# Optimization experiments

Measured on AMD Instinct MI355X. Metric: run time of the kernel, lower is better.

## Reference

```python
import jax, jax.numpy as jnp
import numpy as np

N = 50000   # nodes
E = 600000  # edges
D = 128     # in_channels
H = 32      # MLP hidden


def setup_inputs() -> dict:
    key = jax.random.key(0)
    ks = jax.random.split(key, 10)
    x = jax.random.normal(ks[0], (N, D), dtype=jnp.float32)
    edge_index = jax.random.randint(ks[1], (2, E), 0, N, dtype=jnp.int32)
    W_gcn = jax.random.normal(ks[2], (D, D), dtype=jnp.float32) / np.sqrt(D)
    b_gcn = jnp.zeros((D,), dtype=jnp.float32)
    w1 = jax.random.normal(ks[3], (D, H), dtype=jnp.float32) / np.sqrt(D)
    b1 = jnp.zeros((H,), dtype=jnp.float32)
    w2 = jax.random.normal(ks[4], (H, H), dtype=jnp.float32) / np.sqrt(H)
    b2 = jnp.zeros((H,), dtype=jnp.float32)
    w3 = jax.random.normal(ks[5], (H, 1), dtype=jnp.float32) / np.sqrt(H)
    b3 = jnp.zeros((1,), dtype=jnp.float32)
    return {"x": x, "edge_index": edge_index, "W_gcn": W_gcn, "b_gcn": b_gcn,
            "w1": w1, "b1": b1, "w2": w2, "b2": b2, "w3": w3, "b3": b3}


def _gcn_conv(x, edge_index, W, b):
    """PyG GCNConv: add self-loops, symmetric D^-1/2 (A+I) D^-1/2 normalization."""
    xw = x @ W  # [N, D]
    loop = jnp.arange(N, dtype=edge_index.dtype)
    row = jnp.concatenate([edge_index[0], loop])  # source
    col = jnp.concatenate([edge_index[1], loop])  # target
    deg = jax.ops.segment_sum(jnp.ones_like(col, dtype=xw.dtype), col, num_segments=N)
    dinv = jnp.where(deg > 0, jax.lax.rsqrt(deg), 0.0)
    norm = dinv[row] * dinv[col]              # [E+N]
    msg = xw[row] * norm[:, None]             # gather + scale, [E+N, D]
    out = jax.ops.segment_sum(msg, col, num_segments=N)  # scatter-add, [N, D]
    return out + b


def reference(x, edge_index, W_gcn, b_gcn, w1, b1, w2, b2, w3, b3):
    out = jax.nn.relu(_gcn_conv(x, edge_index, W_gcn, b_gcn))
    h = out + x                               # residual
    h = jax.nn.relu(h @ w1 + b1)
    h = jax.nn.relu(h @ w2 + b2)
    return h @ w3 + b3                        # [N, 1]
```

## Files before the change

### kernel.cpp

```cpp
#include <hip/hip_runtime.h>

#define DIM 128
#define HID 32
#define CAP 64
#define NFILL 512

typedef __attribute__((ext_vector_type(8))) short v8s;
typedef __attribute__((ext_vector_type(8))) unsigned short v8u;
typedef __attribute__((ext_vector_type(4))) float v4f;
typedef __attribute__((ext_vector_type(4))) int v4i;

static __device__ __forceinline__ unsigned short f2bf(float f) {
    unsigned int u = __float_as_uint(f);
    u += 0x7fffu + ((u >> 16) & 1u);
    return (unsigned short)(u >> 16);
}

__global__ __launch_bounds__(256) void prep_kernel(int* __restrict__ cnt,
                                                   const float* __restrict__ W,
                                                   unsigned short* __restrict__ wbt,
                                                   int n) {
    int gtid = (int)blockIdx.x * 256 + threadIdx.x;
    int nthr = (int)gridDim.x * 256;
    for (int i = gtid * 4; i < n; i += nthr * 4) {
        if (i + 3 < n) {
            *(int4*)&cnt[i] = make_int4(0, 0, 0, 0);
        } else {
            for (int k = i; k < n; ++k) cnt[k] = 0;
        }
    }
    for (int f = gtid; f < DIM * DIM; f += nthr) {
        int k = f >> 7, nn = f & 127;
        wbt[nn * 128 + k] = f2bf(W[f]);
    }
}

__global__ __launch_bounds__(256, 4) void gemm_fill_kernel(const float* __restrict__ x,
                                                           const unsigned short* __restrict__ wbt,
                                                           signed char* __restrict__ xwq,
                                                           float* __restrict__ sc,
                                                           const int* __restrict__ ei,
                                                           int* __restrict__ cnt,
                                                           int* __restrict__ srcs,
                                                           int n, int E) {
    int t = threadIdx.x;
    int b = (int)blockIdx.x;
    if (b < NFILL) {
        const int* col = ei + E;
        const int xcd = b & 7;
        const int s = b >> 3;
        const int nslice = NFILL >> 3;
        const int quads = (E + 3) >> 2;
        const int qps = (quads + nslice - 1) / nslice;
        const int q0 = s * qps;
        const int q1 = min(q0 + qps, quads);
        for (int qi = q0 + t; qi < q1; qi += 256) {
            int base = qi * 4;
            if (base + 3 < E) {
                v4i r = __builtin_nontemporal_load((const v4i*)&ei[base]);
                v4i c = __builtin_nontemporal_load((const v4i*)&col[base]);
#pragma unroll
                for (int u = 0; u < 4; ++u) {
                    int cc = c[u];
                    if ((cc & 7) == xcd) {
                        int p = atomicAdd(&cnt[cc], 1);
                        if (p < CAP) srcs[(cc << 6) + p] = r[u];
                    }
                }
            } else {
                for (int e = base; e < E; ++e) {
                    int cc = col[e];
                    if ((cc & 7) == xcd) {
                        int p = atomicAdd(&cnt[cc], 1);
                        if (p < CAP) srcs[(cc << 6) + p] = ei[e];
                    }
                }
            }
        }
    } else {
        int tile = b - NFILL;
        int row0 = tile * 64;
        int w = t >> 6;
        int l = t & 63;
        int q = l >> 4;
        int mn = l & 15;
        int row = row0 + w * 16 + mn;

        v8s afrag[4];
        const float* xr = x + (size_t)row * DIM + q * 8;
#pragma unroll
        for (int kt = 0; kt < 4; ++kt) {
            float4 qa = make_float4(0.f, 0.f, 0.f, 0.f), qb = qa;
            if (row < n) {
                const float4* s4 = (const float4*)(xr + kt * 32);
                qa = s4[0];
                qb = s4[1];
            }
            v8u pk;
            pk[0] = f2bf(qa.x); pk[1] = f2bf(qa.y); pk[2] = f2bf(qa.z); pk[3] = f2bf(qa.w);
            pk[4] = f2bf(qb.x); pk[5] = f2bf(qb.y); pk[6] = f2bf(qb.z); pk[7] = f2bf(qb.w);
            afrag[kt] = (v8s)pk;
        }

        v4f acc[8];
        const unsigned short* wr = wbt + mn * 128 + q * 8;
#pragma unroll
        for (int ct = 0; ct < 8; ++ct) {
            acc[ct] = (v4f){0.f, 0.f, 0.f, 0.f};
#pragma unroll
            for (int kt = 0; kt < 4; ++kt) {
                v8s bfrag = *(const v8s*)(wr + ct * (16 * 128) + kt * 32);
                acc[ct] = __builtin_amdgcn_mfma_f32_16x16x32_bf16(afrag[kt], bfrag, acc[ct], 0, 0, 0);
            }
        }

        float m[4];
#pragma unroll
        for (int i = 0; i < 4; ++i) {
            float mm = 0.f;
#pragma unroll
            for (int ct = 0; ct < 8; ++ct) mm = fmaxf(mm, fabsf(acc[ct][i]));
            m[i] = mm;
        }
#pragma unroll
        for (int off = 1; off < 16; off <<= 1) {
#pragma unroll
            for (int i = 0; i < 4; ++i) m[i] = fmaxf(m[i], __shfl_xor(m[i], off));
        }
        float inv[4];
#pragma unroll
        for (int i = 0; i < 4; ++i) {
            m[i] = fmaxf(m[i], 1e-20f);
            inv[i] = 127.0f / m[i];
        }
        if (mn == 0) {
#pragma unroll
            for (int i = 0; i < 4; ++i) {
                int rowg = row0 + w * 16 + q * 4 + i;
                if (rowg < n) sc[rowg] = m[i] * (1.0f / 127.0f);
            }
        }
#pragma unroll
        for (int ct = 0; ct < 8; ++ct) {
            int colg = ct * 16 + mn;
#pragma unroll
            for (int i = 0; i < 4; ++i) {
                int rowg = row0 + w * 16 + q * 4 + i;
                if (rowg < n)
                    xwq[(size_t)rowg * DIM + colg] =
                        (signed char)__float2int_rn(acc[ct][i] * inv[i]);
            }
        }
    }
}

__global__ __launch_bounds__(256) void gather_tail_kernel(
    const signed char* __restrict__ xwq, const float* __restrict__ x,
    const int* __restrict__ cnt, const int* __restrict__ srcs,
    const float* __restrict__ sc, const float* __restrict__ b_gcn,
    const float* __restrict__ w1, const float* __restrict__ b1,
    const float* __restrict__ w2, const float* __restrict__ b2,
    const float* __restrict__ w3, const float* __restrict__ b3,
    float* __restrict__ out, int n) {
    __shared__ float hs[8][132];
    __shared__ float t1s[8][40];
    int t = threadIdx.x;
    int g = t >> 5, j = t & 31;
    int node = blockIdx.x * 8 + g;

    if (node < n) {
        int d = min(cnt[node], CAP);
        int beg = node << 6;
        int aq = ((const int*)(xwq + (size_t)node * DIM))[j];
        float scn = sc[node];
        float4 xv = ((const float4*)(x + (size_t)node * DIM))[j];
        float4 bg = ((const float4*)b_gcn)[j];
        float ax = 0.f, ay = 0.f, az = 0.f, aw = 0.f;
        for (int c0 = 0; c0 < d; c0 += 32) {
            int sj = 0; float wj = 0.f;
            if (c0 + j < d) {
                sj = srcs[beg + c0 + j];
                wj = rsqrtf((float)cnt[sj] + 1.0f) * sc[sj];
            }
            int m = min(32, d - c0);
            for (int i = 0; i < m; i += 8) {
                int v[8]; float wgt[8];
#pragma unroll
                for (int u = 0; u < 8; ++u) {
                    int src = __shfl(sj, i + u, 32);
                    wgt[u] = __shfl(wj, i + u, 32);
                    v[u] = ((const int*)(xwq + (size_t)src * DIM))[j];
                }
#pragma unroll
                for (int u = 0; u < 8; ++u) {
                    ax += wgt[u] * (float)((v[u] << 24) >> 24);
                    ay += wgt[u] * (float)((v[u] << 16) >> 24);
                    az += wgt[u] * (float)((v[u] <<  8) >> 24);
                    aw += wgt[u] * (float)( v[u]        >> 24);
                }
            }
        }
        float di = rsqrtf((float)d + 1.0f);
        float sself = di * di * scn;
        float* h = &hs[g][4 * j];
        h[0] = fmaxf(di * ax + sself * (float)((aq << 24) >> 24) + bg.x, 0.f) + xv.x;
        h[1] = fmaxf(di * ay + sself * (float)((aq << 16) >> 24) + bg.y, 0.f) + xv.y;
        h[2] = fmaxf(di * az + sself * (float)((aq <<  8) >> 24) + bg.z, 0.f) + xv.z;
        h[3] = fmaxf(di * aw + sself * (float)( aq        >> 24) + bg.w, 0.f) + xv.w;
        float acc = b1[j];
        for (int k = 0; k < DIM; k += 4) {
            float4 hv = *(const float4*)&hs[g][k];
            acc += hv.x * w1[(k + 0) * HID + j];
            acc += hv.y * w1[(k + 1) * HID + j];
            acc += hv.z * w1[(k + 2) * HID + j];
            acc += hv.w * w1[(k + 3) * HID + j];
        }
        t1s[g][j] = fmaxf(acc, 0.0f);
        acc = b2[j];
        for (int k = 0; k < HID; k += 4) {
            float4 tv = *(const float4*)&t1s[g][k];
            acc += tv.x * w2[(k + 0) * HID + j];
            acc += tv.y * w2[(k + 1) * HID + j];
            acc += tv.z * w2[(k + 2) * HID + j];
            acc += tv.w * w2[(k + 3) * HID + j];
        }
        float v = fmaxf(acc, 0.0f) * w3[j];
#pragma unroll
        for (int off = 16; off > 0; off >>= 1) v += __shfl_down(v, off, 32);
        if (j == 0) out[node] = v + b3[0];
    }
}

extern "C" void kernel_launch(void* const* d_in, const int* in_sizes, int n_in,
                              void* d_out, int out_size, void* d_ws, size_t ws_size,
                              hipStream_t stream) {
    const float* x     = (const float*)d_in[0];
    const int*   ei    = (const int*)d_in[1];
    const float* W_gcn = (const float*)d_in[2];
    const float* b_gcn = (const float*)d_in[3];
    const float* w1    = (const float*)d_in[4];
    const float* b1    = (const float*)d_in[5];
    const float* w2    = (const float*)d_in[6];
    const float* b2    = (const float*)d_in[7];
    const float* w3    = (const float*)d_in[8];
    const float* b3    = (const float*)d_in[9];
    float* out = (float*)d_out;

    const int n = in_sizes[0] / DIM;
    const int E = in_sizes[1] / 2;

    char* ws = (char*)d_ws;
    signed char* xwq = (signed char*)ws;
    char* p = ws + (size_t)n * DIM;
    p = (char*)(((size_t)p + 15) & ~(size_t)15);
    float* sc   = (float*)p;         p += (size_t)n * sizeof(float);
    int*   cnt  = (int*)p;           p += (size_t)n * sizeof(int);
    p = (char*)(((size_t)p + 255) & ~(size_t)255);
    int*   srcs = (int*)p;           p += (size_t)n * CAP * sizeof(int);
    unsigned short* wbt = (unsigned short*)p;

    const int ngemm = (n + 63) / 64;

    prep_kernel<<<64, 256, 0, stream>>>(cnt, W_gcn, wbt, n);
    gemm_fill_kernel<<<NFILL + ngemm, 256, 0, stream>>>(x, wbt, xwq, sc, ei,
                                                        cnt, srcs, n, E);
    gather_tail_kernel<<<(n + 7) / 8, 256, 0, stream>>>(xwq, x, cnt, srcs, sc,
                                                        b_gcn, w1, b1, w2, b2,
                                                        w3, b3, out, n);
}
```

Before: 171.1 us.

## Interleave degree count and scale into int2, widen edge loads, raise occupancy

Stores each node's in-degree and quantization scale together as one int2, so the gather kernel gets both for a neighbor with a single 8-byte load instead of two scattered 4-byte loads. The fill loop now handles eight edges per thread with two vector loads per array. The launch-bounds occupancy hint rises to 8 on the gemm and gather kernels. The trade-offs are atomics landing on strided addresses and possible register spills under the tighter occupancy bound.

```diff
diff --git a/kernel.cpp b/kernel.cpp
--- a/kernel.cpp
+++ b/kernel.cpp
@@ -16,17 +16,17 @@
     return (unsigned short)(u >> 16);
 }
 
-__global__ __launch_bounds__(256) void prep_kernel(int* __restrict__ cnt,
+__global__ __launch_bounds__(256) void prep_kernel(int2* __restrict__ csn,
                                                    const float* __restrict__ W,
                                                    unsigned short* __restrict__ wbt,
                                                    int n) {
     int gtid = (int)blockIdx.x * 256 + threadIdx.x;
     int nthr = (int)gridDim.x * 256;
-    for (int i = gtid * 4; i < n; i += nthr * 4) {
-        if (i + 3 < n) {
-            *(int4*)&cnt[i] = make_int4(0, 0, 0, 0);
+    for (int i = gtid * 2; i < n; i += nthr * 2) {
+        if (i + 1 < n) {
+            *(int4*)&csn[i] = make_int4(0, 0, 0, 0);
         } else {
-            for (int k = i; k < n; ++k) cnt[k] = 0;
+            csn[i] = make_int2(0, 0);
         }
     }
     for (int f = gtid; f < DIM * DIM; f += nthr) {
@@ -35,43 +35,53 @@
     }
 }
 
-__global__ __launch_bounds__(256, 4) void gemm_fill_kernel(const float* __restrict__ x,
+__global__ __launch_bounds__(256, 8) void gemm_fill_kernel(const float* __restrict__ x,
                                                            const unsigned short* __restrict__ wbt,
                                                            signed char* __restrict__ xwq,
-                                                           float* __restrict__ sc,
+                                                           int2* __restrict__ csn,
                                                            const int* __restrict__ ei,
-                                                           int* __restrict__ cnt,
                                                            int* __restrict__ srcs,
                                                            int n, int E) {
     int t = threadIdx.x;
     int b = (int)blockIdx.x;
     if (b < NFILL) {
         const int* col = ei + E;
+        int* cnt = (int*)csn;
         const int xcd = b & 7;
         const int s = b >> 3;
         const int nslice = NFILL >> 3;
-        const int quads = (E + 3) >> 2;
-        const int qps = (quads + nslice - 1) / nslice;
-        const int q0 = s * qps;
-        const int q1 = min(q0 + qps, quads);
-        for (int qi = q0 + t; qi < q1; qi += 256) {
-            int base = qi * 4;
-            if (base + 3 < E) {
-                v4i r = __builtin_nontemporal_load((const v4i*)&ei[base]);
-                v4i c = __builtin_nontemporal_load((const v4i*)&col[base]);
+        const int octs = (E + 7) >> 3;
+        const int ops = (octs + nslice - 1) / nslice;
+        const int o0 = s * ops;
+        const int o1 = min(o0 + ops, octs);
+        for (int oi = o0 + t; oi < o1; oi += 256) {
+            int base = oi * 8;
+            if (base + 7 < E) {
+                v4i ra = __builtin_nontemporal_load((const v4i*)&ei[base]);
+                v4i rb = __builtin_nontemporal_load((const v4i*)&ei[base + 4]);
+                v4i ca = __builtin_nontemporal_load((const v4i*)&col[base]);
+                v4i cb = __builtin_nontemporal_load((const v4i*)&col[base + 4]);
 #pragma unroll
                 for (int u = 0; u < 4; ++u) {
-                    int cc = c[u];
+                    int cc = ca[u];
                     if ((cc & 7) == xcd) {
-                        int p = atomicAdd(&cnt[cc], 1);
-                        if (p < CAP) srcs[(cc << 6) + p] = r[u];
+                        int p = atomicAdd(&cnt[cc * 2], 1);
+                        if (p < CAP) srcs[(cc << 6) + p] = ra[u];
+                    }
+                }
+#pragma unroll
+                for (int u = 0; u < 4; ++u) {
+                    int cc = cb[u];
+                    if ((cc & 7) == xcd) {
+                        int p = atomicAdd(&cnt[cc * 2], 1);
+                        if (p < CAP) srcs[(cc << 6) + p] = rb[u];
                     }
                 }
             } else {
                 for (int e = base; e < E; ++e) {
                     int cc = col[e];
                     if ((cc & 7) == xcd) {
-                        int p = atomicAdd(&cnt[cc], 1);
+                        int p = atomicAdd(&cnt[cc * 2], 1);
                         if (p < CAP) srcs[(cc << 6) + p] = ei[e];
                     }
                 }
@@ -137,7 +147,7 @@
 #pragma unroll
             for (int i = 0; i < 4; ++i) {
                 int rowg = row0 + w * 16 + q * 4 + i;
-                if (rowg < n) sc[rowg] = m[i] * (1.0f / 127.0f);
+                if (rowg < n) csn[rowg].y = __float_as_int(m[i] * (1.0f / 127.0f));
             }
         }
 #pragma unroll
@@ -154,10 +164,10 @@
     }
 }
 
-__global__ __launch_bounds__(256) void gather_tail_kernel(
+__global__ __launch_bounds__(256, 8) void gather_tail_kernel(
     const signed char* __restrict__ xwq, const float* __restrict__ x,
-    const int* __restrict__ cnt, const int* __restrict__ srcs,
-    const float* __restrict__ sc, const float* __restrict__ b_gcn,
+    const int2* __restrict__ csn, const int* __restrict__ srcs,
+    const float* __restrict__ b_gcn,
     const float* __restrict__ w1, const float* __restrict__ b1,
     const float* __restrict__ w2, const float* __restrict__ b2,
     const float* __restrict__ w3, const float* __restrict__ b3,
@@ -169,10 +179,11 @@
     int node = blockIdx.x * 8 + g;
 
     if (node < n) {
-        int d = min(cnt[node], CAP);
+        int2 cd = csn[node];
+        int d = min(cd.x, CAP);
+        float scn = __int_as_float(cd.y);
         int beg = node << 6;
         int aq = ((const int*)(xwq + (size_t)node * DIM))[j];
-        float scn = sc[node];
         float4 xv = ((const float4*)(x + (size_t)node * DIM))[j];
         float4 bg = ((const float4*)b_gcn)[j];
         float ax = 0.f, ay = 0.f, az = 0.f, aw = 0.f;
@@ -180,7 +191,8 @@
             int sj = 0; float wj = 0.f;
             if (c0 + j < d) {
                 sj = srcs[beg + c0 + j];
-                wj = rsqrtf((float)cnt[sj] + 1.0f) * sc[sj];
+                int2 cw = csn[sj];
+                wj = rsqrtf((float)cw.x + 1.0f) * __int_as_float(cw.y);
             }
             int m = min(32, d - c0);
             for (int i = 0; i < m; i += 8) {
@@ -253,18 +265,17 @@
     signed char* xwq = (signed char*)ws;
     char* p = ws + (size_t)n * DIM;
     p = (char*)(((size_t)p + 15) & ~(size_t)15);
-    float* sc   = (float*)p;         p += (size_t)n * sizeof(float);
-    int*   cnt  = (int*)p;           p += (size_t)n * sizeof(int);
+    int2* csn = (int2*)p;            p += (size_t)n * sizeof(int2);
     p = (char*)(((size_t)p + 255) & ~(size_t)255);
-    int*   srcs = (int*)p;           p += (size_t)n * CAP * sizeof(int);
+    int*  srcs = (int*)p;            p += (size_t)n * CAP * sizeof(int);
     unsigned short* wbt = (unsigned short*)p;
 
     const int ngemm = (n + 63) / 64;
 
-    prep_kernel<<<64, 256, 0, stream>>>(cnt, W_gcn, wbt, n);
-    gemm_fill_kernel<<<NFILL + ngemm, 256, 0, stream>>>(x, wbt, xwq, sc, ei,
-                                                        cnt, srcs, n, E);
-    gather_tail_kernel<<<(n + 7) / 8, 256, 0, stream>>>(xwq, x, cnt, srcs, sc,
+    prep_kernel<<<64, 256, 0, stream>>>(csn, W_gcn, wbt, n);
+    gemm_fill_kernel<<<NFILL + ngemm, 256, 0, stream>>>(x, wbt, xwq, csn, ei,
+                                                        srcs, n, E);
+    gather_tail_kernel<<<(n + 7) / 8, 256, 0, stream>>>(xwq, x, csn, srcs,
                                                         b_gcn, w1, b1, w2, b2,
                                                         w3, b3, out, n);
 }
```

New measurement: 235.1 us. 1.37x slower.
